# Kernel tuning notes

Hardware: AMD Instinct MI355X
Metric: run time of the kernel (lower is better)

Reference implementation:

```python
import jax, jax.numpy as jnp
import numpy as np
from jax import lax

B, C, H, W = 32, 3, 128, 128
HP, WP = 7, 7          # feature map after 4 stride-2 valid 3x3 convs on 128
GH, GW = 32, 32        # glimpse shape
BN_EPS = 1e-5


def _conv(x, w, b, stride):
    y = lax.conv_general_dilated(x, w, (stride, stride), 'VALID',
                                 dimension_numbers=('NCHW', 'OIHW', 'NCHW'))
    return y + b[None, :, None, None]


def _bn(x, g, be):
    # training-mode BatchNorm2d: biased batch stats over (N,H,W)
    m = x.mean(axis=(0, 2, 3), keepdims=True)
    v = ((x - m) ** 2).mean(axis=(0, 2, 3), keepdims=True)
    return g[None, :, None, None] * (x - m) * lax.rsqrt(v + BN_EPS) + be[None, :, None, None]


def setup_inputs() -> dict:
    key = jax.random.key(0)
    ks = jax.random.split(key, 16)
    def w_init(k, shape):
        fan_in = shape[1] * shape[2] * shape[3]
        return (jax.random.normal(k, shape, jnp.float32) / np.sqrt(fan_in)).astype(jnp.float32)
    chans = [3, 64, 64, 64, 64]
    inp = {}
    inp['img'] = jax.random.normal(ks[0], (B, C, H, W), jnp.float32)
    inp['eps_scale'] = jax.random.normal(ks[1], (B, HP, WP, 2), jnp.float32)
    inp['eps_shift'] = jax.random.normal(ks[2], (B, HP, WP, 2), jnp.float32)
    for i in range(4):
        inp[f'w{i+1}'] = w_init(ks[3 + i], (chans[i + 1], chans[i], 3, 3))
        inp[f'b{i+1}'] = jnp.zeros((chans[i + 1],), jnp.float32)
        inp[f'g{i+1}'] = jnp.ones((chans[i + 1],), jnp.float32)
        inp[f'be{i+1}'] = jnp.zeros((chans[i + 1],), jnp.float32)
    inp['wp'] = w_init(ks[10], (64, 64, 1, 1)); inp['bp'] = jnp.zeros((64,), jnp.float32)
    inp['wz'] = w_init(ks[11], (11, 64, 1, 1)); inp['bz'] = jnp.zeros((11,), jnp.float32)
    return inp


def reference(img, eps_scale, eps_shift,
              w1, b1, g1, be1, w2, b2, g2, be2,
              w3, b3, g3, be3, w4, b4, g4, be4,
              wp, bp, wz, bz):
    h = img
    for (w, b, g, be) in ((w1, b1, g1, be1), (w2, b2, g2, be2),
                          (w3, b3, g3, be3), (w4, b4, g4, be4)):
        h = jax.nn.elu(_bn(_conv(h, w, b, 2), g, be))
    feats = jax.nn.elu(_conv(h, wp, bp, 1))            # [B,64,HP,WP]

    # --- znet and latent splits (only scale/shift affect returned glimpses) ---
    Z = _conv(feats, wz, bz, 1).transpose(0, 2, 3, 1)  # [B,HP,WP,11]
    smean, slogstd = Z[..., 3:5], Z[..., 5:7]
    shmean, shlogstd = Z[..., 7:9], Z[..., 9:11]
    z_scale = smean + jax.nn.softplus(slogstd) * eps_scale
    z_shift = shmean + jax.nn.softplus(shlogstd) * eps_shift

    glimpse_hw = jnp.array([GH, GW], jnp.float32)
    image_hw = jnp.array([H, W], jnp.float32)
    fmap_hw = jnp.array([HP, WP], jnp.float32)
    scale_img = jax.nn.sigmoid(z_scale) * glimpse_hw / image_hw   # [B,HP,WP,2] (h,w)
    shift_img = jax.nn.sigmoid(z_shift) / fmap_hw                 # [B,HP,WP,2] (i,j)

    ii = jnp.arange(HP, dtype=jnp.float32) / HP
    jj = jnp.arange(WP, dtype=jnp.float32) / WP
    ij = jnp.stack(jnp.meshgrid(ii, jj, indexing='ij'), axis=-1)  # [HP,WP,2]
    center = (ij[None] + shift_img) * 2.0 - 1.0                   # [B,HP,WP,2] in [-1,1]

    K = HP * WP
    th = scale_img[..., 0].reshape(B, K)   # height scale
    tw = scale_img[..., 1].reshape(B, K)   # width scale
    tx = center[..., 0].reshape(B, K)      # row (y) center
    ty = center[..., 1].reshape(B, K)      # col (x) center

    # affine_grid (align_corners=False) base coords; theta = [[tw,0,ty],[0,th,tx]]
    xb = (2.0 * jnp.arange(GW, dtype=jnp.float32) + 1.0) / GW - 1.0
    yb = (2.0 * jnp.arange(GH, dtype=jnp.float32) + 1.0) / GH - 1.0
    ixn = tw[:, :, None, None] * xb[None, None, None, :] + ty[:, :, None, None]  # [B,K,1,GW]
    iyn = th[:, :, None, None] * yb[None, None, :, None] + tx[:, :, None, None]  # [B,K,GH,1]
    # normalized -> pixel coords (align_corners=False)
    px = jnp.broadcast_to(((ixn + 1.0) * W - 1.0) * 0.5, (B, K, GH, GW))
    py = jnp.broadcast_to(((iyn + 1.0) * H - 1.0) * 0.5, (B, K, GH, GW))

    def sample_one(im, pxb, pyb):
        # im [C,H,W]; pxb/pyb [K,GH,GW]; bilinear, zero padding
        x0 = jnp.floor(pxb); y0 = jnp.floor(pyb)
        wx1 = pxb - x0; wy1 = pyb - y0
        x0i = x0.astype(jnp.int32); y0i = y0.astype(jnp.int32)
        x1i = x0i + 1; y1i = y0i + 1
        def g(yi, xi):
            m = ((xi >= 0) & (xi < W) & (yi >= 0) & (yi < H)).astype(im.dtype)
            v = im[:, jnp.clip(yi, 0, H - 1), jnp.clip(xi, 0, W - 1)]  # [C,K,GH,GW]
            return v * m[None]
        return (g(y0i, x0i) * ((1 - wy1) * (1 - wx1))[None]
                + g(y0i, x1i) * ((1 - wy1) * wx1)[None]
                + g(y1i, x0i) * (wy1 * (1 - wx1))[None]
                + g(y1i, x1i) * (wy1 * wx1)[None])

    xs = jax.vmap(sample_one)(img, px, py)            # [B,C,K,GH,GW]
    return xs.transpose(0, 2, 1, 3, 4).reshape(B * K, C, GH, GW)
```

## Files before the change

### kernel.cpp

```cpp
#include <hip/hip_runtime.h>
#include <math.h>

#define BATCH 32

__device__ __forceinline__ float eluf(float v) { return v > 0.f ? v : expm1f(v); }
__device__ __forceinline__ float softplusf(float x) {
    return fmaxf(x, 0.f) + log1pf(expf(-fabsf(x)));
}
__device__ __forceinline__ float sigmoidf(float x) { return 1.f / (1.f + expf(-x)); }

template <int CIN, int HIN, int WIN, int HOUT, int WOUT, int PAIRS, int BLOCK>
__global__ __launch_bounds__(BLOCK, 4) void conv_kernel(
    const float* __restrict__ in, const float* __restrict__ w, const float* __restrict__ bias,
    float* __restrict__ out, float* __restrict__ stats)
{
    constexpr int NW = BLOCK / 64;
    __shared__ float red_s[NW][8];
    __shared__ float red_q[NW][8];

    const int b   = blockIdx.x;
    const int co0 = blockIdx.y * 8;
    const int t   = threadIdx.x;

    const int xw_r  = t % WOUT;
    const int pr_r  = t / WOUT;
    const bool active = pr_r < PAIRS;
    const int pr = active ? pr_r : 0;
    const int xw = active ? xw_r : 0;
    const int y0 = (blockIdx.z * PAIRS + pr) * 2;
    const bool row1 = (y0 + 1) < HOUT;

    int roff[5];
#pragma unroll
    for (int r = 0; r < 5; ++r)
        roff[r] = min(2 * y0 + r, HIN - 1) * WIN + 2 * xw;

    const float* ib = in + (size_t)b * CIN * HIN * WIN;

    float acc0[8], acc1[8];
#pragma unroll
    for (int u = 0; u < 8; ++u) { acc0[u] = bias[co0 + u]; acc1[u] = bias[co0 + u]; }

#pragma unroll 2
    for (int ci = 0; ci < CIN; ++ci) {
        const float* ip = ib + (size_t)ci * (HIN * WIN);
        float pch[15];
#pragma unroll
        for (int r = 0; r < 5; ++r)
#pragma unroll
            for (int c = 0; c < 3; ++c)
                pch[r * 3 + c] = ip[roff[r] + c];

        const float* wc = w + ((size_t)co0 * CIN + ci) * 9;
#pragma unroll
        for (int u = 0; u < 8; ++u)
#pragma unroll
            for (int j = 0; j < 9; ++j) {
                const float wv = wc[u * CIN * 9 + j];
                acc0[u] = fmaf(pch[j],     wv, acc0[u]);
                acc1[u] = fmaf(pch[6 + j], wv, acc1[u]);
            }
    }

    const int lane = t & 63, wv_ = t >> 6;
#pragma unroll
    for (int u = 0; u < 8; ++u) {
        float v0 = active ? acc0[u] : 0.f;
        float v1 = (active && row1) ? acc1[u] : 0.f;
        if (active) {
            float* op = out + (((size_t)b * 64 + co0 + u) * HOUT + y0) * WOUT + xw;
            op[0] = v0;
            if (row1) op[WOUT] = v1;
        }
        float s = v0 + v1, q = v0 * v0 + v1 * v1;
#pragma unroll
        for (int off = 32; off > 0; off >>= 1) {
            s += __shfl_down(s, off);
            q += __shfl_down(q, off);
        }
        if (lane == 0) { red_s[wv_][u] = s; red_q[wv_][u] = q; }
    }
    __syncthreads();
    if (t < 16) {
        const int u = t >> 1, which = t & 1;
        float tt = 0.f;
#pragma unroll
        for (int k = 0; k < NW; ++k) tt += which ? red_q[k][u] : red_s[k][u];
        atomicAdd(&stats[2 * (co0 + u) + which], tt);
    }
}

template <int PLANE>
__global__ __launch_bounds__(256) void bnelu_kernel(
    float* __restrict__ h, const float* __restrict__ stats,
    const float* __restrict__ g, const float* __restrict__ be)
{
    const float invN = 1.f / (float)(BATCH * PLANE);
    const long long total = (long long)BATCH * 64 * PLANE;
    for (long long idx = (long long)blockIdx.x * blockDim.x + threadIdx.x; idx < total;
         idx += (long long)gridDim.x * blockDim.x) {
        int c = (int)((idx / PLANE) & 63);
        float s = stats[2 * c], q = stats[2 * c + 1];
        float m = s * invN;
        float var = fmaf(q, invN, -m * m);
        float a = g[c] * rsqrtf(var + 1e-5f);
        float bb = fmaf(-a, m, be[c]);
        h[idx] = eluf(fmaf(a, h[idx], bb));
    }
}

__global__ __launch_bounds__(256) void head_kernel(
    const float* __restrict__ x4, const float* __restrict__ stats4,
    const float* __restrict__ g4, const float* __restrict__ be4,
    const float* __restrict__ wp, const float* __restrict__ bp,
    const float* __restrict__ wz, const float* __restrict__ bz,
    const float* __restrict__ eps_scale, const float* __restrict__ eps_shift,
    float* __restrict__ params)
{
    __shared__ float xs[64 * 49];
    __shared__ float fe[64 * 49];
    __shared__ float zz[11 * 49];
    __shared__ float ha[64], hb[64];
    const int b = blockIdx.x, t = threadIdx.x;

    if (t < 64) {
        constexpr float invN = 1.f / (float)(BATCH * 49);
        float s = stats4[2 * t], q = stats4[2 * t + 1];
        float m = s * invN;
        float var = fmaf(q, invN, -m * m);
        float a = g4[t] * rsqrtf(var + 1e-5f);
        ha[t] = a;
        hb[t] = fmaf(-a, m, be4[t]);
    }
    __syncthreads();

    for (int i = t; i < 64 * 49; i += 256) {
        int c = i / 49;
        xs[i] = eluf(fmaf(ha[c], x4[(size_t)b * 64 * 49 + i], hb[c]));
    }
    __syncthreads();

    for (int i = t; i < 64 * 49; i += 256) {
        int co = i / 49, p = i % 49;
        float a = bp[co];
        for (int ci = 0; ci < 64; ++ci) a = fmaf(xs[ci * 49 + p], wp[co * 64 + ci], a);
        fe[i] = eluf(a);
    }
    __syncthreads();

    for (int i = t; i < 11 * 49; i += 256) {
        int co = i / 49, p = i % 49;
        float a = bz[co];
        for (int ci = 0; ci < 64; ++ci) a = fmaf(fe[ci * 49 + p], wz[co * 64 + ci], a);
        zz[i] = a;
    }
    __syncthreads();

    if (t < 49) {
        const int i = t / 7, j = t % 7;
        float es0 = eps_scale[((size_t)b * 49 + t) * 2 + 0];
        float es1 = eps_scale[((size_t)b * 49 + t) * 2 + 1];
        float eh0 = eps_shift[((size_t)b * 49 + t) * 2 + 0];
        float eh1 = eps_shift[((size_t)b * 49 + t) * 2 + 1];
        float zs0 = zz[3 * 49 + t] + softplusf(zz[5 * 49 + t]) * es0;
        float zs1 = zz[4 * 49 + t] + softplusf(zz[6 * 49 + t]) * es1;
        float zh0 = zz[7 * 49 + t] + softplusf(zz[9 * 49 + t]) * eh0;
        float zh1 = zz[8 * 49 + t] + softplusf(zz[10 * 49 + t]) * eh1;
        float th = sigmoidf(zs0) * 0.25f;
        float tw = sigmoidf(zs1) * 0.25f;
        float tx = ((float)i / 7.0f + sigmoidf(zh0) / 7.0f) * 2.f - 1.f;
        float ty = ((float)j / 7.0f + sigmoidf(zh1) / 7.0f) * 2.f - 1.f;
        float4* pp = (float4*)params;
        pp[b * 49 + t] = make_float4(th, tw, tx, ty);
    }
}

__device__ __forceinline__ float tap(const float* __restrict__ im, int yy, int xx) {
    bool ok = (xx >= 0) & (xx < 128) & (yy >= 0) & (yy < 128);
    int yc = min(max(yy, 0), 127);
    int xc = min(max(xx, 0), 127);
    return ok ? im[yc * 128 + xc] : 0.f;
}

__global__ __launch_bounds__(256) void sampler_kernel(
    const float* __restrict__ img, const float* __restrict__ params,
    float* __restrict__ out)
{
    const int bk = blockIdx.x;
    const int b  = bk / 49;
    const float4 pr = ((const float4*)params)[bk];
    const float th = pr.x, tw = pr.y, tx = pr.z, ty = pr.w;

    for (int idx = threadIdx.x; idx < 3072; idx += 256) {
        const int c  = idx >> 10;
        const int gy = (idx >> 5) & 31;
        const int gx = idx & 31;
        float xb = (2.f * gx + 1.f) / 32.f - 1.f;
        float yb = (2.f * gy + 1.f) / 32.f - 1.f;
        float ixn = fmaf(tw, xb, ty);
        float iyn = fmaf(th, yb, tx);
        float px = ((ixn + 1.f) * 128.f - 1.f) * 0.5f;
        float py = ((iyn + 1.f) * 128.f - 1.f) * 0.5f;
        float x0f = floorf(px), y0f = floorf(py);
        float wx = px - x0f, wy = py - y0f;
        int x0 = (int)x0f, y0 = (int)y0f;
        const float* im = img + ((size_t)b * 3 + c) * 16384;
        float v00 = tap(im, y0, x0);
        float v01 = tap(im, y0, x0 + 1);
        float v10 = tap(im, y0 + 1, x0);
        float v11 = tap(im, y0 + 1, x0 + 1);
        float r = v00 * (1.f - wy) * (1.f - wx) + v01 * (1.f - wy) * wx +
                  v10 * wy * (1.f - wx)        + v11 * wy * wx;
        out[(size_t)bk * 3072 + idx] = r;
    }
}

extern "C" void kernel_launch(void* const* d_in, const int* in_sizes, int n_in,
                              void* d_out, int out_size, void* d_ws, size_t ws_size,
                              hipStream_t stream)
{
    const float* img       = (const float*)d_in[0];
    const float* eps_scale = (const float*)d_in[1];
    const float* eps_shift = (const float*)d_in[2];
    const float* w1 = (const float*)d_in[3],  *b1 = (const float*)d_in[4];
    const float* g1 = (const float*)d_in[5],  *be1 = (const float*)d_in[6];
    const float* w2 = (const float*)d_in[7],  *b2 = (const float*)d_in[8];
    const float* g2 = (const float*)d_in[9],  *be2 = (const float*)d_in[10];
    const float* w3 = (const float*)d_in[11], *b3 = (const float*)d_in[12];
    const float* g3 = (const float*)d_in[13], *be3 = (const float*)d_in[14];
    const float* w4 = (const float*)d_in[15], *b4 = (const float*)d_in[16];
    const float* g4 = (const float*)d_in[17], *be4 = (const float*)d_in[18];
    const float* wp = (const float*)d_in[19], *bp = (const float*)d_in[20];
    const float* wz = (const float*)d_in[21], *bz = (const float*)d_in[22];

    float* ws     = (float*)d_ws;
    float* stats  = ws;
    float* params = ws + 512;
    float* h1     = ws + 6784;
    float* h2     = h1 + (size_t)32 * 64 * 63 * 63;
    float* h3     = h2 + (size_t)32 * 64 * 31 * 31;
    float* h4     = h3 + (size_t)32 * 64 * 15 * 15;

    float* outp = (float*)d_out;

    hipMemsetAsync(stats, 0, 512 * sizeof(float), stream);

    conv_kernel<3, 128, 128, 63, 63, 4, 256>
        <<<dim3(32, 8, 8), 256, 0, stream>>>(img, w1, b1, h1, stats + 0);
    bnelu_kernel<63 * 63><<<2048, 256, 0, stream>>>(h1, stats + 0, g1, be1);

    conv_kernel<64, 63, 63, 31, 31, 8, 256>
        <<<dim3(32, 8, 2), 256, 0, stream>>>(h1, w2, b2, h2, stats + 128);
    bnelu_kernel<31 * 31><<<2048, 256, 0, stream>>>(h2, stats + 128, g2, be2);

    conv_kernel<64, 31, 31, 15, 15, 8, 128>
        <<<dim3(32, 8, 1), 128, 0, stream>>>(h2, w3, b3, h3, stats + 256);
    bnelu_kernel<15 * 15><<<1024, 256, 0, stream>>>(h3, stats + 256, g3, be3);

    conv_kernel<64, 15, 15, 7, 7, 4, 64>
        <<<dim3(32, 8, 1), 64, 0, stream>>>(h3, w4, b4, h4, stats + 384);

    head_kernel<<<32, 256, 0, stream>>>(h4, stats + 384, g4, be4, wp, bp, wz, bz,
                                        eps_scale, eps_shift, params);

    sampler_kernel<<<1568, 256, 0, stream>>>(img, params, outp);
}
```

Baseline: 232.9 us.

## Use one output pixel per thread with per-layer channel group sizes in convs

The conv kernel now computes a single output pixel per thread instead of a vertical pair of rows. The number of output channels per block becomes a template parameter G, set per layer (8, 4, 2, 1), and the launch grids grow to match. The aim is to raise parallelism and occupancy in the small deep layers (the launch bounds hint goes from 4 to 8 blocks). The cost is losing the shared-row reuse between paired outputs, so more input loads per FMA, plus more atomics for the BN statistics.

```diff
diff --git a/kernel.cpp b/kernel.cpp
--- a/kernel.cpp
+++ b/kernel.cpp
@@ -9,70 +9,54 @@
 }
 __device__ __forceinline__ float sigmoidf(float x) { return 1.f / (1.f + expf(-x)); }
 
-template <int CIN, int HIN, int WIN, int HOUT, int WOUT, int PAIRS, int BLOCK>
-__global__ __launch_bounds__(BLOCK, 4) void conv_kernel(
+template <int CIN, int HIN, int WIN, int HOUT, int WOUT, int G, int BLOCK>
+__global__ __launch_bounds__(BLOCK, 8) void conv_kernel(
     const float* __restrict__ in, const float* __restrict__ w, const float* __restrict__ bias,
     float* __restrict__ out, float* __restrict__ stats)
 {
     constexpr int NW = BLOCK / 64;
-    __shared__ float red_s[NW][8];
-    __shared__ float red_q[NW][8];
+    __shared__ float red_s[NW][G];
+    __shared__ float red_q[NW][G];
 
     const int b   = blockIdx.x;
-    const int co0 = blockIdx.y * 8;
+    const int co0 = blockIdx.y * G;
     const int t   = threadIdx.x;
-
-    const int xw_r  = t % WOUT;
-    const int pr_r  = t / WOUT;
-    const bool active = pr_r < PAIRS;
-    const int pr = active ? pr_r : 0;
-    const int xw = active ? xw_r : 0;
-    const int y0 = (blockIdx.z * PAIRS + pr) * 2;
-    const bool row1 = (y0 + 1) < HOUT;
-
-    int roff[5];
-#pragma unroll
-    for (int r = 0; r < 5; ++r)
-        roff[r] = min(2 * y0 + r, HIN - 1) * WIN + 2 * xw;
-
-    const float* ib = in + (size_t)b * CIN * HIN * WIN;
-
-    float acc0[8], acc1[8];
-#pragma unroll
-    for (int u = 0; u < 8; ++u) { acc0[u] = bias[co0 + u]; acc1[u] = bias[co0 + u]; }
+    const int px  = blockIdx.z * BLOCK + t;
+    const bool active = px < HOUT * WOUT;
+    const int p = active ? px : 0;
+    const int y = p / WOUT, x = p % WOUT;
+
+    const float* ib = in + (size_t)b * CIN * HIN * WIN + (2 * y) * WIN + 2 * x;
+
+    float acc[G];
+#pragma unroll
+    for (int u = 0; u < G; ++u) acc[u] = bias[co0 + u];
 
 #pragma unroll 2
     for (int ci = 0; ci < CIN; ++ci) {
         const float* ip = ib + (size_t)ci * (HIN * WIN);
-        float pch[15];
-#pragma unroll
-        for (int r = 0; r < 5; ++r)
-#pragma unroll
-            for (int c = 0; c < 3; ++c)
-                pch[r * 3 + c] = ip[roff[r] + c];
+        float pch[9];
+#pragma unroll
+        for (int ky = 0; ky < 3; ++ky)
+#pragma unroll
+            for (int kx = 0; kx < 3; ++kx)
+                pch[ky * 3 + kx] = ip[ky * WIN + kx];
 
         const float* wc = w + ((size_t)co0 * CIN + ci) * 9;
 #pragma unroll
-        for (int u = 0; u < 8; ++u)
-#pragma unroll
-            for (int j = 0; j < 9; ++j) {
-                const float wv = wc[u * CIN * 9 + j];
-                acc0[u] = fmaf(pch[j],     wv, acc0[u]);
-                acc1[u] = fmaf(pch[6 + j], wv, acc1[u]);
-            }
+        for (int u = 0; u < G; ++u)
+#pragma unroll
+            for (int j = 0; j < 9; ++j)
+                acc[u] = fmaf(pch[j], wc[u * CIN * 9 + j], acc[u]);
     }
 
     const int lane = t & 63, wv_ = t >> 6;
 #pragma unroll
-    for (int u = 0; u < 8; ++u) {
-        float v0 = active ? acc0[u] : 0.f;
-        float v1 = (active && row1) ? acc1[u] : 0.f;
-        if (active) {
-            float* op = out + (((size_t)b * 64 + co0 + u) * HOUT + y0) * WOUT + xw;
-            op[0] = v0;
-            if (row1) op[WOUT] = v1;
-        }
-        float s = v0 + v1, q = v0 * v0 + v1 * v1;
+    for (int u = 0; u < G; ++u) {
+        float v = active ? acc[u] : 0.f;
+        if (active)
+            out[(((size_t)b * 64 + co0 + u) * HOUT + y) * WOUT + x] = v;
+        float s = v, q = v * v;
 #pragma unroll
         for (int off = 32; off > 0; off >>= 1) {
             s += __shfl_down(s, off);
@@ -81,7 +65,7 @@
         if (lane == 0) { red_s[wv_][u] = s; red_q[wv_][u] = q; }
     }
     __syncthreads();
-    if (t < 16) {
+    if (t < 2 * G) {
         const int u = t >> 1, which = t & 1;
         float tt = 0.f;
 #pragma unroll
@@ -245,20 +229,20 @@
 
     hipMemsetAsync(stats, 0, 512 * sizeof(float), stream);
 
-    conv_kernel<3, 128, 128, 63, 63, 4, 256>
-        <<<dim3(32, 8, 8), 256, 0, stream>>>(img, w1, b1, h1, stats + 0);
+    conv_kernel<3, 128, 128, 63, 63, 8, 256>
+        <<<dim3(32, 8, 16), 256, 0, stream>>>(img, w1, b1, h1, stats + 0);
     bnelu_kernel<63 * 63><<<2048, 256, 0, stream>>>(h1, stats + 0, g1, be1);
 
-    conv_kernel<64, 63, 63, 31, 31, 8, 256>
-        <<<dim3(32, 8, 2), 256, 0, stream>>>(h1, w2, b2, h2, stats + 128);
+    conv_kernel<64, 63, 63, 31, 31, 4, 256>
+        <<<dim3(32, 16, 4), 256, 0, stream>>>(h1, w2, b2, h2, stats + 128);
     bnelu_kernel<31 * 31><<<2048, 256, 0, stream>>>(h2, stats + 128, g2, be2);
 
-    conv_kernel<64, 31, 31, 15, 15, 8, 128>
-        <<<dim3(32, 8, 1), 128, 0, stream>>>(h2, w3, b3, h3, stats + 256);
+    conv_kernel<64, 31, 31, 15, 15, 2, 256>
+        <<<dim3(32, 32, 1), 256, 0, stream>>>(h2, w3, b3, h3, stats + 256);
     bnelu_kernel<15 * 15><<<1024, 256, 0, stream>>>(h3, stats + 256, g3, be3);
 
-    conv_kernel<64, 15, 15, 7, 7, 4, 64>
-        <<<dim3(32, 8, 1), 64, 0, stream>>>(h3, w4, b4, h4, stats + 384);
+    conv_kernel<64, 15, 15, 7, 7, 1, 64>
+        <<<dim3(32, 64, 1), 64, 0, stream>>>(h3, w4, b4, h4, stats + 384);
 
     head_kernel<<<32, 256, 0, stream>>>(h4, stats + 384, g4, be4, wp, bp, wz, bz,
                                         eps_scale, eps_shift, params);
```

New measurement: 205.0 us. 12.0% less time.
